# Performance work log

Hardware: AMD Instinct MI355X
Metric: run time of the kernel (lower is better)

The kernel has to match this reference:

```python
import jax, jax.numpy as jnp
import numpy as np

HEADS = 4
DIM_HEAD = 32
SCALE = DIM_HEAD ** -0.5


def setup_inputs() -> dict:
    key = jax.random.key(0)
    ks = jax.random.split(key, 6)
    B, C, H, W = 4, 256, 64, 64
    inner = HEADS * DIM_HEAD  # 128
    x = jax.random.normal(ks[0], (B, C, H, W), dtype=jnp.float32)
    s_in = 1.0 / np.sqrt(C)
    s_inner = 1.0 / np.sqrt(inner)
    Wq = jax.random.normal(ks[1], (inner, C), dtype=jnp.float32) * s_in
    Wk = jax.random.normal(ks[2], (inner, C), dtype=jnp.float32) * s_in
    Wv = jax.random.normal(ks[3], (inner, C), dtype=jnp.float32) * s_in
    Wout = jax.random.normal(ks[4], (C, inner), dtype=jnp.float32) * s_inner
    bout = jnp.zeros((C,), dtype=jnp.float32)
    return {"x": x, "Wq": Wq, "Wk": Wk, "Wv": Wv, "Wout": Wout, "bout": bout}


def reference(x, Wq, Wk, Wv, Wout, bout):
    b, c, h, w = x.shape
    n = h * w
    xf = x.reshape(b, c, n)  # b c n
    # 1x1 convs (no bias) == channel matmuls
    q = jnp.einsum('oc,bcn->bon', Wq, xf)
    k = jnp.einsum('oc,bcn->bon', Wk, xf)
    v = jnp.einsum('oc,bcn->bon', Wv, xf)
    # split heads: b (h d) n -> b h d n
    q = q.reshape(b, HEADS, DIM_HEAD, n) * SCALE
    k = k.reshape(b, HEADS, DIM_HEAD, n)
    v = v.reshape(b, HEADS, DIM_HEAD, n)
    qk = jnp.einsum('bhdi,bhdj->bhij', q, k)  # [b, h, n, n]
    attn = jax.nn.softmax(qk, axis=-1)  # stable (max-subtracted), matches original
    att_val = jnp.einsum('bhij,bhdj->bhid', attn, v)  # [b, h, n, d]
    # b h (x y) d -> b (h d) x y
    out = att_val.transpose(0, 1, 3, 2).reshape(b, HEADS * DIM_HEAD, h, w)
    # final 1x1 conv with bias
    out = jnp.einsum('oc,bcxy->boxy', Wout, out) + bout[None, :, None, None]
    return out
```

## Files before the change

kernel.cpp:

```cpp
#include <hip/hip_runtime.h>
#include <hip/hip_fp16.h>
#include <math.h>

typedef _Float16 f16x8 __attribute__((ext_vector_type(8)));
typedef float    f32x4 __attribute__((ext_vector_type(4)));
typedef unsigned int u32x4 __attribute__((ext_vector_type(4)));
typedef unsigned short u16;
typedef unsigned int   u32;

#define MFMA_F16(a, b, c) __builtin_amdgcn_mfma_f32_16x16x32_f16((a), (b), (c), 0, 0, 0)

#define NSP 4096
#define QK_SCALE (0.17677669529663687f * 1.4426950408889634f)

__device__ __forceinline__ float fexp2(float x) {
#if __has_builtin(__builtin_amdgcn_exp2f)
  return __builtin_amdgcn_exp2f(x);
#else
  return exp2f(x);
#endif
}

__device__ __forceinline__ u32 pk_f16(float a, float b) {
#if __has_builtin(__builtin_amdgcn_cvt_pkrtz)
  return __builtin_bit_cast(u32, __builtin_amdgcn_cvt_pkrtz(a, b));
#else
  u16 lo = __builtin_bit_cast(u16, (_Float16)a);
  u16 hi = __builtin_bit_cast(u16, (_Float16)b);
  return (u32)lo | ((u32)hi << 16);
#endif
}

__device__ __forceinline__ u16 f16bits(float a) {
  return __builtin_bit_cast(u16, (_Float16)a);
}

__device__ __forceinline__ float f16val(u16 v) {
  return (float)__builtin_bit_cast(_Float16, v);
}

__global__ __launch_bounds__(512) void qkv_proj_kernel(
    const float* __restrict__ x, const float* __restrict__ Wq,
    const float* __restrict__ Wk, const float* __restrict__ Wv,
    u16* __restrict__ Qo, u16* __restrict__ Ko, u16* __restrict__ Vo)
{
  const int b  = blockIdx.y;
  const int j0 = blockIdx.x * 64;
  const int tid  = threadIdx.x;
  const int wave = tid >> 6, lane = tid & 63;
  const int g = lane >> 4, r = lane & 15;
  const float* xb = x + (size_t)b * 256 * NSP;

  const f32x4 ZERO4 = {0.f, 0.f, 0.f, 0.f};
  f32x4 acc[3][4];
#pragma unroll
  for (int m = 0; m < 3; ++m)
#pragma unroll
    for (int n = 0; n < 4; ++n) acc[m][n] = ZERO4;

  for (int kc = 0; kc < 8; ++kc) {
    f16x8 bfrag[4];
#pragma unroll
    for (int nt = 0; nt < 4; ++nt) {
      const float* src = xb + (size_t)(kc * 32 + g * 8) * NSP + j0 + nt * 16 + r;
      f16x8 f;
#pragma unroll
      for (int i = 0; i < 8; ++i) f[i] = (_Float16)src[(size_t)i * NSP];
      bfrag[nt] = f;
    }
#pragma unroll
    for (int mm = 0; mm < 3; ++mm) {
      const int o_tile = wave * 48 + mm * 16;
      const float* wsrc = (o_tile < 128) ? Wq : ((o_tile < 256) ? Wk : Wv);
      const float* arow = wsrc + ((o_tile & 127) + r) * 256 + kc * 32 + g * 8;
      f16x8 af;
#pragma unroll
      for (int i = 0; i < 8; ++i) af[i] = (_Float16)arow[i];
#pragma unroll
      for (int nt = 0; nt < 4; ++nt)
        acc[mm][nt] = MFMA_F16(af, bfrag[nt], acc[mm][nt]);
    }
  }

#pragma unroll
  for (int mm = 0; mm < 3; ++mm) {
    const int o_tile = wave * 48 + mm * 16;
    const int part = o_tile >> 7;
    const int o_in = o_tile & 127;
    const int head = o_in >> 5;
    const int dbase = (o_in & 31) + g * 4;
#pragma unroll
    for (int nt = 0; nt < 4; ++nt) {
      const int j = j0 + nt * 16 + r;
      if (part < 2) {
        u16* dst = (part == 0) ? Qo : Ko;
        const float sc = (part == 0) ? QK_SCALE : 1.0f;
        const size_t base = ((size_t)((b * 4 + head) * NSP + j)) * 32 + dbase;
        const u32 p01 = pk_f16(acc[mm][nt][0] * sc, acc[mm][nt][1] * sc);
        const u32 p23 = pk_f16(acc[mm][nt][2] * sc, acc[mm][nt][3] * sc);
        *(u32*)(dst + base)     = p01;
        *(u32*)(dst + base + 2) = p23;
      } else {
        const int jb = j & ~31, off = j & 31;
        const int s = (((off >> 2) & 3) << 3) | (((off >> 4) & 1) << 2) | (off & 3);
#pragma unroll
        for (int i = 0; i < 4; ++i)
          Vo[((size_t)((b * 4 + head) * 32 + dbase + i)) * NSP + jb + s] =
              f16bits(acc[mm][nt][i]);
      }
    }
  }
}

__global__ __launch_bounds__(256, 2) void attn_kernel(
    const u16* __restrict__ Qg, const u16* __restrict__ Kg,
    const u16* __restrict__ Vg, u32* __restrict__ P32,
    float* __restrict__ mlp)
{
  const int d    = blockIdx.x;
  const int bh   = (d & 7) * 2 + ((d >> 3) & 1);
  const int hf   = (d >> 4) & 1;
  const int qt   = d >> 5;
  const int wave = threadIdx.x >> 6, lane = threadIdx.x & 63;
  const int g = lane >> 4, r = lane & 15;
  const int q0 = qt * 256 + wave * 64;
  const int kvbase = hf * 2048;

  const size_t qkb = (size_t)bh * NSP * 32;
  const u16* Kp = Kg + qkb;
  const u16* Vp = Vg + (size_t)bh * 32 * NSP;

  const f16x8 qf0 = *(const f16x8*)(Qg + qkb + (size_t)(q0 + r) * 32 + g * 8);
  const f16x8 qf1 = *(const f16x8*)(Qg + qkb + (size_t)(q0 + 16 + r) * 32 + g * 8);
  const f16x8 qf2 = *(const f16x8*)(Qg + qkb + (size_t)(q0 + 32 + r) * 32 + g * 8);
  const f16x8 qf3 = *(const f16x8*)(Qg + qkb + (size_t)(q0 + 48 + r) * 32 + g * 8);

  const f32x4 ZERO4 = {0.f, 0.f, 0.f, 0.f};
  f32x4 Oc00 = ZERO4, Oc01 = ZERO4, Oc10 = ZERO4, Oc11 = ZERO4;
  f32x4 Oc20 = ZERO4, Oc21 = ZERO4, Oc30 = ZERO4, Oc31 = ZERO4;
  f32x4 lacc0 = ZERO4, lacc1 = ZERO4, lacc2 = ZERO4, lacc3 = ZERO4;
  f32x4 mC0 = ZERO4, mC1 = ZERO4, mC2 = ZERO4, mC3 = ZERO4;
  float mrun0 = 0.0f, mrun1 = 0.0f, mrun2 = 0.0f, mrun3 = 0.0f;

  f16x8 ones;
#pragma unroll
  for (int i = 0; i < 8; ++i) ones[i] = (_Float16)1.0f;

  const u16* kptr  = Kp + (size_t)(kvbase + r) * 32 + g * 8;
  const u16* vptr0 = Vp + (size_t)r * NSP + kvbase + g * 8;
  const u16* vptr1 = vptr0 + (size_t)16 * NSP;

  f16x8 kfA0, kfA1, kfA2, kfA3, kfB0, kfB1, kfB2, kfB3;
#define LOADK(d0, d1, d2, d3)                                                 \
  {                                                                           \
    d0 = *(const f16x8*)(kptr);                                               \
    d1 = *(const f16x8*)(kptr + 512);                                         \
    d2 = *(const f16x8*)(kptr + 1024);                                        \
    d3 = *(const f16x8*)(kptr + 1536);                                        \
    kptr += 2048;                                                             \
  }

  LOADK(kfA0, kfA1, kfA2, kfA3);

#define PLMAX(PM, Sa, Sb, Sc, Sd)                                             \
  {                                                                           \
    float x0 = fmaxf(fmaxf(Sa[0], Sa[1]), Sa[2]);                             \
    float x1 = fmaxf(fmaxf(Sa[3], Sb[0]), Sb[1]);                             \
    float x2 = fmaxf(fmaxf(Sb[2], Sb[3]), Sc[0]);                             \
    float x3 = fmaxf(fmaxf(Sc[1], Sc[2]), Sc[3]);                             \
    float x4 = fmaxf(fmaxf(Sd[0], Sd[1]), Sd[2]);                             \
    PM = fmaxf(fmaxf(fmaxf(x0, x1), x2), fmaxf(fmaxf(x3, x4), Sd[3]));        \
  }

#define RESCALE(PM, MRUN, MC, Sa, Sb, Sc, Sd, OA, OB, LA)                     \
  {                                                                           \
    float tm = fmaxf(PM, __shfl_xor(PM, 16));                                 \
    tm = fmaxf(tm, __shfl_xor(tm, 32));                                       \
    const float dd = fmaxf(tm, 0.0f);                                         \
    const float al = fexp2(-dd);                                              \
    MRUN += dd;                                                               \
    MC[0] -= dd; MC[1] -= dd; MC[2] -= dd; MC[3] -= dd;                       \
    Sa[0] -= dd; Sa[1] -= dd; Sa[2] -= dd; Sa[3] -= dd;                       \
    Sb[0] -= dd; Sb[1] -= dd; Sb[2] -= dd; Sb[3] -= dd;                       \
    Sc[0] -= dd; Sc[1] -= dd; Sc[2] -= dd; Sc[3] -= dd;                       \
    Sd[0] -= dd; Sd[1] -= dd; Sd[2] -= dd; Sd[3] -= dd;                       \
    OA[0] *= al; OA[1] *= al; OA[2] *= al; OA[3] *= al;                       \
    OB[0] *= al; OB[1] *= al; OB[2] *= al; OB[3] *= al;                       \
    LA[0] *= al; LA[1] *= al; LA[2] *= al; LA[3] *= al;                       \
  }

#define PACK_PV(Sa, Sb, Sc, Sd, OA, OB, LA)                                   \
  {                                                                           \
    u32x4 w0, w1;                                                             \
    w0[0] = pk_f16(fexp2(Sa[0]), fexp2(Sa[1]));                               \
    w0[1] = pk_f16(fexp2(Sa[2]), fexp2(Sa[3]));                               \
    w0[2] = pk_f16(fexp2(Sb[0]), fexp2(Sb[1]));                               \
    w0[3] = pk_f16(fexp2(Sb[2]), fexp2(Sb[3]));                               \
    w1[0] = pk_f16(fexp2(Sc[0]), fexp2(Sc[1]));                               \
    w1[1] = pk_f16(fexp2(Sc[2]), fexp2(Sc[3]));                               \
    w1[2] = pk_f16(fexp2(Sd[0]), fexp2(Sd[1]));                               \
    w1[3] = pk_f16(fexp2(Sd[2]), fexp2(Sd[3]));                               \
    const f16x8 pB0 = __builtin_bit_cast(f16x8, w0);                          \
    const f16x8 pB1 = __builtin_bit_cast(f16x8, w1);                          \
    OA = MFMA_F16(vf00, pB0, OA);                                             \
    OB = MFMA_F16(vf10, pB0, OB);                                             \
    LA = MFMA_F16(ones, pB0, LA);                                             \
    OA = MFMA_F16(vf01, pB1, OA);                                             \
    OB = MFMA_F16(vf11, pB1, OB);                                             \
    LA = MFMA_F16(ones, pB1, LA);                                             \
  }

#define PROCESS(K0, K1, K2, K3, PREFETCH)                                     \
  {                                                                           \
    const f16x8 vf00 = *(const f16x8*)(vptr0);                                \
    const f16x8 vf01 = *(const f16x8*)(vptr0 + 32);                           \
    const f16x8 vf10 = *(const f16x8*)(vptr1);                                \
    const f16x8 vf11 = *(const f16x8*)(vptr1 + 32);                           \
    vptr0 += 64; vptr1 += 64;                                                 \
    PREFETCH;                                                                 \
    f32x4 S00 = MFMA_F16(K0, qf0, mC0);                                       \
    f32x4 S01 = MFMA_F16(K1, qf0, mC0);                                       \
    f32x4 S02 = MFMA_F16(K2, qf0, mC0);                                       \
    f32x4 S03 = MFMA_F16(K3, qf0, mC0);                                       \
    f32x4 S10 = MFMA_F16(K0, qf1, mC1);                                       \
    f32x4 S11 = MFMA_F16(K1, qf1, mC1);                                       \
    f32x4 S12 = MFMA_F16(K2, qf1, mC1);                                       \
    f32x4 S13 = MFMA_F16(K3, qf1, mC1);                                       \
    f32x4 S20 = MFMA_F16(K0, qf2, mC2);                                       \
    f32x4 S21 = MFMA_F16(K1, qf2, mC2);                                       \
    f32x4 S22 = MFMA_F16(K2, qf2, mC2);                                       \
    f32x4 S23 = MFMA_F16(K3, qf2, mC2);                                       \
    f32x4 S30 = MFMA_F16(K0, qf3, mC3);                                       \
    f32x4 S31 = MFMA_F16(K1, qf3, mC3);                                       \
    f32x4 S32 = MFMA_F16(K2, qf3, mC3);                                       \
    f32x4 S33 = MFMA_F16(K3, qf3, mC3);                                       \
    float pm0, pm1, pm2, pm3;                                                 \
    PLMAX(pm0, S00, S01, S02, S03);                                           \
    PLMAX(pm1, S10, S11, S12, S13);                                           \
    PLMAX(pm2, S20, S21, S22, S23);                                           \
    PLMAX(pm3, S30, S31, S32, S33);                                           \
    if (__any((pm0 > 8.0f) || (pm1 > 8.0f) || (pm2 > 8.0f) || (pm3 > 8.0f))) {\
      RESCALE(pm0, mrun0, mC0, S00, S01, S02, S03, Oc00, Oc01, lacc0);        \
      RESCALE(pm1, mrun1, mC1, S10, S11, S12, S13, Oc10, Oc11, lacc1);        \
      RESCALE(pm2, mrun2, mC2, S20, S21, S22, S23, Oc20, Oc21, lacc2);        \
      RESCALE(pm3, mrun3, mC3, S30, S31, S32, S33, Oc30, Oc31, lacc3);        \
    }                                                                         \
    PACK_PV(S00, S01, S02, S03, Oc00, Oc01, lacc0);                           \
    PACK_PV(S10, S11, S12, S13, Oc10, Oc11, lacc1);                           \
    PACK_PV(S20, S21, S22, S23, Oc20, Oc21, lacc2);                           \
    PACK_PV(S30, S31, S32, S33, Oc30, Oc31, lacc3);                           \
  }

  for (int tt = 0; tt < 32; tt += 2) {
    PROCESS(kfA0, kfA1, kfA2, kfA3, LOADK(kfB0, kfB1, kfB2, kfB3));
    if (tt + 2 < 32) {
      PROCESS(kfB0, kfB1, kfB2, kfB3, LOADK(kfA0, kfA1, kfA2, kfA3));
    } else {
      PROCESS(kfB0, kfB1, kfB2, kfB3, );
    }
  }
#undef PROCESS
#undef LOADK
#undef PLMAX
#undef RESCALE
#undef PACK_PV

  const int b = bh >> 2, h = bh & 3;
  const int rowb = b * 256 + hf * 64 + h * 16;
  const int sb = b * 8 + hf * 4 + h;

#define EPI(OA, OB, LA, MR, QOFF)                                             \
  {                                                                           \
    const float inv = 1.0f / LA[0];                                           \
    const int q = q0 + (QOFF) + r;                                            \
    P32[(size_t)(rowb + g * 2)     * 4096 + q] =                              \
        pk_f16(OA[0] * inv, OA[1] * inv);                                     \
    P32[(size_t)(rowb + g * 2 + 1) * 4096 + q] =                              \
        pk_f16(OA[2] * inv, OA[3] * inv);                                     \
    P32[(size_t)(rowb + 8 + g * 2)     * 4096 + q] =                          \
        pk_f16(OB[0] * inv, OB[1] * inv);                                     \
    P32[(size_t)(rowb + 8 + g * 2 + 1) * 4096 + q] =                          \
        pk_f16(OB[2] * inv, OB[3] * inv);                                     \
    if (g == 0) {                                                             \
      const size_t mlb = ((size_t)sb * 2) * 4096 + q;                         \
      mlp[mlb] = MR;                                                          \
      mlp[mlb + 4096] = LA[0];                                                \
    }                                                                         \
  }

  EPI(Oc00, Oc01, lacc0, mrun0, 0);
  EPI(Oc10, Oc11, lacc1, mrun1, 16);
  EPI(Oc20, Oc21, lacc2, mrun2, 32);
  EPI(Oc30, Oc31, lacc3, mrun3, 48);
#undef EPI
}

__global__ __launch_bounds__(512) void outproj_kernel(
    const float* __restrict__ Wout, const float* __restrict__ bout,
    const float* __restrict__ mlp, float* __restrict__ out)
{
  __shared__ u16 A_lds[64][136];
  const int j0  = blockIdx.x * 64;
  const int b   = blockIdx.y;
  const int tid = threadIdx.x;
  const int wave = tid >> 6, lane = tid & 63;
  const int g = lane >> 4, r = lane & 15;

  {
    const int jl = lane;
    const int j = j0 + jl;
    const int ch0 = wave * 16;
    const int h = ch0 >> 5;
    const size_t mb0 = ((size_t)((b * 8 + h) * 2)) * 4096 + j;
    const size_t mb1 = ((size_t)((b * 8 + 4 + h) * 2)) * 4096 + j;
    const float m0 = mlp[mb0], l0 = mlp[mb0 + 4096];
    const float m1 = mlp[mb1], l1 = mlp[mb1 + 4096];
    const float M = fmaxf(m0, m1);
    float w0 = l0 * fexp2(m0 - M);
    float w1 = l1 * fexp2(m1 - M);
    const float winv = 1.0f / (w0 + w1);
    w0 *= winv; w1 *= winv;

    const u32* O32 = (const u32*)out;
#pragma unroll
    for (int k2 = 0; k2 < 8; ++k2) {
      const int ch = ch0 + k2 * 2;
      const int dv2 = (ch & 31) >> 1;
      const u32 v0 = O32[(size_t)(b * 256 + h * 16 + dv2) * 4096 + j];
      const u32 v1 = O32[(size_t)(b * 256 + 64 + h * 16 + dv2) * 4096 + j];
      const float e0 = w0 * f16val((u16)(v0 & 0xffff)) +
                       w1 * f16val((u16)(v1 & 0xffff));
      const float e1 = w0 * f16val((u16)(v0 >> 16)) +
                       w1 * f16val((u16)(v1 >> 16));
      *(u32*)&A_lds[jl][ch] = pk_f16(e0, e1);
    }
  }
  __syncthreads();

  const int o0 = wave * 32;
  f32x4 acc[2][4];
#pragma unroll
  for (int mt = 0; mt < 2; ++mt) {
    const float* bp = bout + o0 + mt * 16 + g * 4;
    const f32x4 bias = *(const f32x4*)bp;
#pragma unroll
    for (int nt = 0; nt < 4; ++nt) acc[mt][nt] = bias;
  }

#pragma unroll
  for (int kc = 0; kc < 4; ++kc) {
    f16x8 af[2];
#pragma unroll
    for (int mt = 0; mt < 2; ++mt) {
      const float* wr = Wout + (size_t)(o0 + mt * 16 + r) * 128 + kc * 32 + g * 8;
      const f32x4 wa = *(const f32x4*)(wr);
      const f32x4 wb = *(const f32x4*)(wr + 4);
      u32x4 wp;
      wp[0] = pk_f16(wa[0], wa[1]);
      wp[1] = pk_f16(wa[2], wa[3]);
      wp[2] = pk_f16(wb[0], wb[1]);
      wp[3] = pk_f16(wb[2], wb[3]);
      af[mt] = __builtin_bit_cast(f16x8, wp);
    }
    f16x8 bf[4];
#pragma unroll
    for (int nt = 0; nt < 4; ++nt)
      bf[nt] = *(const f16x8*)&A_lds[nt * 16 + r][kc * 32 + g * 8];
#pragma unroll
    for (int mt = 0; mt < 2; ++mt)
#pragma unroll
      for (int nt = 0; nt < 4; ++nt)
        acc[mt][nt] = MFMA_F16(af[mt], bf[nt], acc[mt][nt]);
  }

#pragma unroll
  for (int mt = 0; mt < 2; ++mt)
#pragma unroll
    for (int nt = 0; nt < 4; ++nt) {
      const int j = j0 + nt * 16 + r;
#pragma unroll
      for (int i = 0; i < 4; ++i) {
        const int o = o0 + mt * 16 + g * 4 + i;
        out[((size_t)(b * 256 + o)) * 4096 + j] = acc[mt][nt][i];
      }
    }
}

extern "C" void kernel_launch(void* const* d_in, const int* in_sizes, int n_in,
                              void* d_out, int out_size, void* d_ws, size_t ws_size,
                              hipStream_t stream) {
  const float* x    = (const float*)d_in[0];
  const float* Wq   = (const float*)d_in[1];
  const float* Wk   = (const float*)d_in[2];
  const float* Wv   = (const float*)d_in[3];
  const float* Wout = (const float*)d_in[4];
  const float* bout = (const float*)d_in[5];
  float* out = (float*)d_out;

  char* ws = (char*)d_ws;
  u16*   Qw = (u16*)(ws);
  u16*   Kw = (u16*)(ws + (4u << 20));
  u16*   Vw = (u16*)(ws + (8u << 20));
  float* ml = (float*)(ws + (12u << 20));

  qkv_proj_kernel<<<dim3(64, 4), 512, 0, stream>>>(x, Wq, Wk, Wv, Qw, Kw, Vw);
  attn_kernel<<<dim3(512), 256, 0, stream>>>(Qw, Kw, Vw, (u32*)out, ml);
  outproj_kernel<<<dim3(64, 4), 512, 0, stream>>>(Wout, bout, ml, out);
}
```

Baseline: 81.91 us.

## Split attention KV range into four chunks instead of two

The attention kernel now splits each query tile's key/value range into four 1024-key partitions instead of two, doubling the grid to 1024 blocks. Each block processes half as many KV tiles. The output-projection kernel merges four partial results using their stored max and sum statistics. This is meant to fill the GPU better (512 blocks on 256 CUs at two blocks per CU is a single wave), at the cost of more partial-output traffic and a heavier merge step.

```diff
diff --git a/kernel.cpp b/kernel.cpp
--- a/kernel.cpp
+++ b/kernel.cpp
@@ -119,12 +119,12 @@
 {
   const int d    = blockIdx.x;
   const int bh   = (d & 7) * 2 + ((d >> 3) & 1);
-  const int hf   = (d >> 4) & 1;
-  const int qt   = d >> 5;
+  const int hf   = (d >> 4) & 3;
+  const int qt   = d >> 6;
   const int wave = threadIdx.x >> 6, lane = threadIdx.x & 63;
   const int g = lane >> 4, r = lane & 15;
   const int q0 = qt * 256 + wave * 64;
-  const int kvbase = hf * 2048;
+  const int kvbase = hf * 1024;
 
   const size_t qkb = (size_t)bh * NSP * 32;
   const u16* Kp = Kg + qkb;
@@ -251,9 +251,9 @@
     PACK_PV(S30, S31, S32, S33, Oc30, Oc31, lacc3);                           \
   }
 
-  for (int tt = 0; tt < 32; tt += 2) {
+  for (int tt = 0; tt < 16; tt += 2) {
     PROCESS(kfA0, kfA1, kfA2, kfA3, LOADK(kfB0, kfB1, kfB2, kfB3));
-    if (tt + 2 < 32) {
+    if (tt + 2 < 16) {
       PROCESS(kfB0, kfB1, kfB2, kfB3, LOADK(kfA0, kfA1, kfA2, kfA3));
     } else {
       PROCESS(kfB0, kfB1, kfB2, kfB3, );
@@ -267,7 +267,7 @@
 
   const int b = bh >> 2, h = bh & 3;
   const int rowb = b * 256 + hf * 64 + h * 16;
-  const int sb = b * 8 + hf * 4 + h;
+  const int sb = b * 16 + hf * 4 + h;
 
 #define EPI(OA, OB, LA, MR, QOFF)                                             \
   {                                                                           \
@@ -311,27 +311,37 @@
     const int j = j0 + jl;
     const int ch0 = wave * 16;
     const int h = ch0 >> 5;
-    const size_t mb0 = ((size_t)((b * 8 + h) * 2)) * 4096 + j;
-    const size_t mb1 = ((size_t)((b * 8 + 4 + h) * 2)) * 4096 + j;
-    const float m0 = mlp[mb0], l0 = mlp[mb0 + 4096];
-    const float m1 = mlp[mb1], l1 = mlp[mb1 + 4096];
-    const float M = fmaxf(m0, m1);
-    float w0 = l0 * fexp2(m0 - M);
-    float w1 = l1 * fexp2(m1 - M);
-    const float winv = 1.0f / (w0 + w1);
-    w0 *= winv; w1 *= winv;
+    float mm[4], ll[4];
+#pragma unroll
+    for (int hf = 0; hf < 4; ++hf) {
+      const size_t mb = ((size_t)((b * 16 + hf * 4 + h) * 2)) * 4096 + j;
+      mm[hf] = mlp[mb];
+      ll[hf] = mlp[mb + 4096];
+    }
+    const float M = fmaxf(fmaxf(mm[0], mm[1]), fmaxf(mm[2], mm[3]));
+    float w[4];
+    float wsum = 0.f;
+#pragma unroll
+    for (int hf = 0; hf < 4; ++hf) {
+      w[hf] = ll[hf] * fexp2(mm[hf] - M);
+      wsum += w[hf];
+    }
+    const float winv = 1.0f / wsum;
+#pragma unroll
+    for (int hf = 0; hf < 4; ++hf) w[hf] *= winv;
 
     const u32* O32 = (const u32*)out;
 #pragma unroll
     for (int k2 = 0; k2 < 8; ++k2) {
       const int ch = ch0 + k2 * 2;
       const int dv2 = (ch & 31) >> 1;
-      const u32 v0 = O32[(size_t)(b * 256 + h * 16 + dv2) * 4096 + j];
-      const u32 v1 = O32[(size_t)(b * 256 + 64 + h * 16 + dv2) * 4096 + j];
-      const float e0 = w0 * f16val((u16)(v0 & 0xffff)) +
-                       w1 * f16val((u16)(v1 & 0xffff));
-      const float e1 = w0 * f16val((u16)(v0 >> 16)) +
-                       w1 * f16val((u16)(v1 >> 16));
+      float e0 = 0.f, e1 = 0.f;
+#pragma unroll
+      for (int hf = 0; hf < 4; ++hf) {
+        const u32 v = O32[(size_t)(b * 256 + hf * 64 + h * 16 + dv2) * 4096 + j];
+        e0 += w[hf] * f16val((u16)(v & 0xffff));
+        e1 += w[hf] * f16val((u16)(v >> 16));
+      }
       *(u32*)&A_lds[jl][ch] = pk_f16(e0, e1);
     }
   }
@@ -404,6 +414,6 @@
   float* ml = (float*)(ws + (12u << 20));
 
   qkv_proj_kernel<<<dim3(64, 4), 512, 0, stream>>>(x, Wq, Wk, Wv, Qw, Kw, Vw);
-  attn_kernel<<<dim3(512), 256, 0, stream>>>(Qw, Kw, Vw, (u32*)out, ml);
+  attn_kernel<<<dim3(1024), 256, 0, stream>>>(Qw, Kw, Vw, (u32*)out, ml);
   outproj_kernel<<<dim3(64, 4), 512, 0, stream>>>(Wout, bout, ml, out);
 }
```

Result: slower. 86.63 us (+5.8%).
